# Kernel optimization log

Measured on AMD Instinct MI355X. Metric: run time of the kernel, lower is better.

## Reference

```python
import jax, jax.numpy as jnp
import numpy as np

E = 8      # num_expert
D = 1024   # d_model
H = 2048   # expert hidden (htoh4 size)
K = 2      # top_k
N = 2048   # tokens (batch*seq)


def setup_inputs() -> dict:
    key = jax.random.key(0)
    ks = jax.random.split(key, 4)
    sc = lambda k, shape, s: jax.random.normal(k, shape, jnp.float32) * s
    return {
        "inp": jax.random.normal(ks[0], (N, D), jnp.float32),
        "Wg": sc(ks[1], (D, E), D ** -0.5),          # NaiveGate linear
        "bg": jnp.zeros((E,), jnp.float32),
        "W1": sc(ks[2], (E, D, H), D ** -0.5),        # per-expert htoh4
        "b1": jnp.zeros((E, H), jnp.float32),
        "W2": sc(ks[3], (E, H, D), H ** -0.5),        # per-expert h4toh
        "b2": jnp.zeros((E, D), jnp.float32),
    }


def reference(inp, Wg, bg, W1, b1, W2, b2):
    # NaiveGate: linear -> top_k logits -> softmax over the k selected logits
    logits = inp @ Wg + bg                              # [N, E]
    top_val, top_idx = jax.lax.top_k(logits, K)         # [N, K]
    gate_score = jax.nn.softmax(top_val, axis=-1)       # [N, K]

    # Expert grouped compute. Reference computes every expert on every token
    # (exact math, no capacity dropping); combine selects the routed ones.
    h = jax.nn.gelu(jnp.einsum('nd,edh->neh', inp, W1) + b1)   # [N, E, H]
    y = jnp.einsum('neh,ehd->ned', h, W2) + b2                 # [N, E, D]

    # Combine: equivalent to bmm(gate_score[N,1,K], x[N,K,D]) after gather.
    comb = jnp.sum(jax.nn.one_hot(top_idx, E, dtype=inp.dtype)
                   * gate_score[..., None], axis=1)            # [N, E]
    return jnp.einsum('ne,ned->nd', comb, y)                   # [N, D]
```

## Files before the change

### kernel.cpp

```cpp
#include <hip/hip_runtime.h>
#include <math.h>

#define N_TOK 2048
#define DM    1024
#define HD    2048
#define NE    8
#define RMAX  5120
#define TMAX  40
#define KSPL  2

#define GATE_BLKS 512
#define XCVT_BLKS 1024
#define PREP_BLKS (GATE_BLKS + XCVT_BLKS)
#define WCV2_BLKS 512

typedef short short8 __attribute__((ext_vector_type(8)));
typedef unsigned short u16x8 __attribute__((ext_vector_type(8)));
typedef float f32x4  __attribute__((ext_vector_type(4)));

__device__ inline unsigned short f2b(float f) {
  unsigned int u = __float_as_uint(f);
  return (unsigned short)((u + 0x7FFFu + ((u >> 16) & 1u)) >> 16);
}
__device__ inline float b2f(unsigned short s) {
  return __uint_as_float(((unsigned int)s) << 16);
}
__device__ inline void gload_lds16(const void* g, void* l) {
  __builtin_amdgcn_global_load_lds(
      (const __attribute__((address_space(1))) unsigned int*)g,
      (__attribute__((address_space(3))) unsigned int*)l, 16, 0, 0);
}

__global__ __launch_bounds__(256) void prep_kernel(
    const float* __restrict__ inp, const float* __restrict__ Wg,
    const float* __restrict__ bg,
    int* __restrict__ top_idx, float* __restrict__ gate_w,
    unsigned short* __restrict__ Xb) {
  int bid = blockIdx.x;
  if (bid < GATE_BLKS) {
    int wave = threadIdx.x >> 6;
    int lane = threadIdx.x & 63;
    int n = bid * 4 + wave;
    float acc[NE];
#pragma unroll
    for (int e = 0; e < NE; ++e) acc[e] = 0.f;
    const float4* wg4 = reinterpret_cast<const float4*>(Wg);
#pragma unroll
    for (int i = 0; i < DM / 64; ++i) {
      int d = i * 64 + lane;
      float x = inp[n * DM + d];
      float4 w0 = wg4[d * 2 + 0];
      float4 w1 = wg4[d * 2 + 1];
      acc[0] += x * w0.x; acc[1] += x * w0.y; acc[2] += x * w0.z; acc[3] += x * w0.w;
      acc[4] += x * w1.x; acc[5] += x * w1.y; acc[6] += x * w1.z; acc[7] += x * w1.w;
    }
#pragma unroll
    for (int off = 32; off > 0; off >>= 1) {
#pragma unroll
      for (int e = 0; e < NE; ++e) acc[e] += __shfl_xor(acc[e], off);
    }
    if (lane == 0) {
      float v0 = -1e30f, v1 = -1e30f; int i0 = -1, i1 = -1;
#pragma unroll
      for (int e = 0; e < NE; ++e) {
        float v = acc[e] + bg[e];
        if (v > v0)      { v1 = v0; i1 = i0; v0 = v; i0 = e; }
        else if (v > v1) { v1 = v;  i1 = e; }
      }
      float e1 = expf(v1 - v0);
      float s  = 1.f + e1;
      top_idx[n * 2]     = i0;
      top_idx[n * 2 + 1] = i1;
      gate_w[n * 2]      = 1.f / s;
      gate_w[n * 2 + 1]  = e1 / s;
    }
  } else {
    int i = ((bid - GATE_BLKS) * 256 + threadIdx.x) * 8;
    float4 a = *(const float4*)(inp + i);
    float4 b = *(const float4*)(inp + i + 4);
    ushort4 pa, pb;
    pa.x = f2b(a.x); pa.y = f2b(a.y); pa.z = f2b(a.z); pa.w = f2b(a.w);
    pb.x = f2b(b.x); pb.y = f2b(b.y); pb.z = f2b(b.z); pb.w = f2b(b.w);
    *(ushort4*)(Xb + i)     = pa;
    *(ushort4*)(Xb + i + 4) = pb;
  }
}

__global__ __launch_bounds__(1024) void group_kernel(
    const int* __restrict__ top_idx,
    const float* __restrict__ W2,
    int* __restrict__ token_of, int* __restrict__ inv_g,
    int* __restrict__ tile_expert, int* __restrict__ tile_row0,
    int* __restrict__ n_tiles,
    unsigned short* __restrict__ W2C) {
  if (blockIdx.x != 0) {
    int wb = blockIdx.x - 1;
    int z  = wb >> 6;
    int k0 = (wb & 63) * 32;
    const float* src = W2 + (size_t)z * HD * DM;
    unsigned short* dst = W2C + (size_t)z * HD * DM;
    int t  = threadIdx.x;
    int cg = t & 255, kg = t >> 8;
    const float* s = src + (size_t)(k0 + kg * 8) * DM + cg * 4;
    float4 v[8];
#pragma unroll
    for (int i = 0; i < 8; ++i) v[i] = *(const float4*)(s + (size_t)i * DM);
#pragma unroll
    for (int c = 0; c < 4; ++c) {
      u16x8 o;
      o[0] = f2b(v[0][c]); o[1] = f2b(v[1][c]); o[2] = f2b(v[2][c]); o[3] = f2b(v[3][c]);
      o[4] = f2b(v[4][c]); o[5] = f2b(v[5][c]); o[6] = f2b(v[6][c]); o[7] = f2b(v[7][c]);
      *(u16x8*)(dst + ((size_t)(k0 / 8 + kg) * DM + cg * 4 + c) * 8) = o;
    }
    return;
  }
  __shared__ int s_wtot[16];
  int tid = threadIdx.x, lane = tid & 63, wid = tid >> 6;
  int base = 0, tiles = 0;
  for (int e = 0; e < NE; ++e) {
    int cnt = 0;
#pragma unroll
    for (int c0 = 0; c0 < N_TOK; c0 += 1024) {
      int n = c0 + tid;
      int t0 = top_idx[n * 2], t1 = top_idx[n * 2 + 1];
      bool f = (t0 == e) || (t1 == e);
      int k = (t0 == e) ? 0 : 1;
      unsigned long long m = __ballot(f);
      int lp = __popcll(m & ((1ull << lane) - 1ull));
      if (lane == 0) s_wtot[wid] = __popcll(m);
      __syncthreads();
      int wbase = 0, tot = 0;
#pragma unroll
      for (int w = 0; w < 16; ++w) {
        int c = s_wtot[w];
        if (w < wid) wbase += c;
        tot += c;
      }
      if (f) {
        int pos = base + cnt + wbase + lp;
        token_of[pos] = n;
        inv_g[n * 2 + k] = pos;
      }
      cnt += tot;
      __syncthreads();
    }
    int padded = (cnt + 127) & ~127;
    for (int i = cnt + tid; i < padded; i += 1024) token_of[base + i] = -1;
    if (tid == 0) {
      for (int t = 0; t < padded / 128; ++t) {
        tile_expert[tiles + t] = e;
        tile_row0[tiles + t]   = base + t * 128;
      }
    }
    tiles += padded / 128;
    base  += padded;
    __syncthreads();
  }
  if (tid == 0) n_tiles[0] = tiles;
}

__global__ __launch_bounds__(256, 6) void ffn1_mfma(
    const unsigned short* __restrict__ Xb,
    const float* __restrict__ W1,
    const float* __restrict__ b1,
    const unsigned short* __restrict__ Xzero,
    const int* __restrict__ token_of, const int* __restrict__ tile_expert,
    const int* __restrict__ tile_row0, const int* __restrict__ n_tiles,
    unsigned short* __restrict__ Hbuf) {
  int lin  = blockIdx.x;
  int xcd  = lin & 7, slot = lin >> 3;
  int unit = xcd * 4 + slot / TMAX;
  int t    = slot % TMAX;
  if (t >= n_tiles[0]) return;
  int e    = tile_expert[t];
  int row0 = tile_row0[t];
  int h0   = unit * 64;
  __shared__ __align__(16) unsigned short Asl[2][128][32];
  __shared__ __align__(16) unsigned short Bsl[2][4][64][8];
  int tid = threadIdx.x, lane = tid & 63;
  int wid = tid >> 6, wr = wid >> 1, wc = wid & 1;
  int l15 = lane & 15, l4 = lane >> 4;
  int sw  = (l15 >> 1) & 3;

  int ar[2], asg[2], tk[2];
#pragma unroll
  for (int q = 0; q < 2; ++q) {
    int idx = tid + q * 256;
    ar[q]  = idx >> 2;
    asg[q] = (idx & 3) ^ ((ar[q] >> 1) & 3);
    tk[q]  = token_of[row0 + ar[q]];
  }
  int bcol = tid & 63, bks = tid >> 6;
  const float* W1e = W1 + (size_t)e * DM * HD;

  f32x4 acc[4][2] = {};
  float bvA[8], bvB[8];

  auto issueB = [&](int tt, float* bv) {
    const float* p = W1e + (size_t)(tt * 32 + bks * 8) * HD + h0 + bcol;
#pragma unroll
    for (int i = 0; i < 8; ++i) bv[i] = p[(size_t)i * HD];
  };
  auto packwrite = [&](const float* bv, int buf) {
    u16x8 o;
#pragma unroll
    for (int i = 0; i < 8; ++i) o[i] = f2b(bv[i]);
    *(u16x8*)&Bsl[buf][bks][bcol][0] = o;
  };
  auto issueA = [&](int tt, int buf) {
#pragma unroll
    for (int q = 0; q < 2; ++q) {
      int idx = tid + q * 256;
      const unsigned short* ga = (tk[q] < 0)
          ? Xzero
          : Xb + (size_t)tk[q] * DM + tt * 32 + asg[q] * 8;
      gload_lds16(ga, (char*)&Asl[buf][0][0] + (size_t)idx * 16);
    }
  };
  auto compute = [&](int buf) {
    short8 a[4], b[2];
#pragma unroll
    for (int m = 0; m < 4; ++m) {
      int R = wr * 64 + m * 16 + l15;
      a[m] = *(const short8*)((const char*)&Asl[buf][0][0] + R * 64 + ((l4 ^ sw) << 4));
    }
#pragma unroll
    for (int n = 0; n < 2; ++n)
      b[n] = *(const short8*)&Bsl[buf][l4][wc * 32 + n * 16 + l15][0];
#pragma unroll
    for (int m = 0; m < 4; ++m)
#pragma unroll
      for (int n = 0; n < 2; ++n)
        acc[m][n] = __builtin_amdgcn_mfma_f32_16x16x32_bf16(a[m], b[n], acc[m][n], 0, 0, 0);
  };

  issueB(0, bvA);
  issueA(0, 0);
  for (int kt = 0; kt < 32; kt += 2) {
    packwrite(bvA, 0);
    __syncthreads();
    if (kt + 1 < 32) { issueB(kt + 1, bvB); issueA(kt + 1, 1); }
    compute(0);
    packwrite(bvB, 1);
    __syncthreads();
    if (kt + 2 < 32) { issueB(kt + 2, bvA); issueA(kt + 2, 0); }
    compute(1);
  }

  float bias[2];
#pragma unroll
  for (int n = 0; n < 2; ++n) bias[n] = b1[e * HD + h0 + wc * 32 + n * 16 + l15];
#pragma unroll
  for (int m = 0; m < 4; ++m) {
#pragma unroll
    for (int n = 0; n < 2; ++n) {
      int col = h0 + wc * 32 + n * 16 + l15;
#pragma unroll
      for (int j = 0; j < 4; ++j) {
        int row = row0 + wr * 64 + m * 16 + l4 * 4 + j;
        float x = acc[m][n][j] + bias[n];
        float g = 0.5f * x * (1.f + tanhf(0.7978845608f * (x + 0.044715f * x * x * x)));
        Hbuf[(size_t)row * HD + col] = f2b(g);
      }
    }
  }
}

__global__ __launch_bounds__(256, 6) void ffn2_mfma(
    const unsigned short* __restrict__ Hbuf,
    const unsigned short* __restrict__ W2C,
    const float* __restrict__ b2,
    const int* __restrict__ tile_expert, const int* __restrict__ tile_row0,
    const int* __restrict__ n_tiles,
    float* __restrict__ Ypart) {
  int lin  = blockIdx.x;
  int xcd  = lin & 7, slot = lin >> 3;
  int unit = xcd * 4 + slot / TMAX;
  int t    = slot % TMAX;
  if (t >= n_tiles[0]) return;
  int e    = tile_expert[t];
  int row0 = tile_row0[t];
  int d0   = (unit >> 1) * 64;
  int ks   = unit & 1;
  int kbase = ks * (HD / KSPL);
  int kb0   = kbase >> 3;
  __shared__ __align__(16) unsigned short Asl[2][128][32];
  __shared__ __align__(16) unsigned short Bsl[2][4][64][8];
  int tid = threadIdx.x, lane = tid & 63;
  int wid = tid >> 6, wr = wid >> 1, wc = wid & 1;
  int l15 = lane & 15, l4 = lane >> 4;
  int sw  = (l15 >> 1) & 3;

  int ar[2], asg[2];
#pragma unroll
  for (int q = 0; q < 2; ++q) {
    int idx = tid + q * 256;
    ar[q]  = idx >> 2;
    asg[q] = (idx & 3) ^ ((ar[q] >> 1) & 3);
  }
  int bcol = tid & 63, bks = tid >> 6;
  const unsigned short* W2e = W2C + (size_t)e * HD * DM;

  f32x4 acc[4][2] = {};

  auto issueAB = [&](int tt, int buf) {
#pragma unroll
    for (int q = 0; q < 2; ++q) {
      int idx = tid + q * 256;
      const unsigned short* ga =
          Hbuf + (size_t)(row0 + ar[q]) * HD + kbase + tt * 32 + asg[q] * 8;
      gload_lds16(ga, (char*)&Asl[buf][0][0] + (size_t)idx * 16);
    }
    const unsigned short* gb =
        W2e + ((size_t)(kb0 + tt * 4 + bks) * DM + d0 + bcol) * 8;
    gload_lds16(gb, (char*)&Bsl[buf][0][0] + (size_t)tid * 16);
  };
  auto compute = [&](int buf) {
    short8 a[4], b[2];
#pragma unroll
    for (int m = 0; m < 4; ++m) {
      int R = wr * 64 + m * 16 + l15;
      a[m] = *(const short8*)((const char*)&Asl[buf][0][0] + R * 64 + ((l4 ^ sw) << 4));
    }
#pragma unroll
    for (int n = 0; n < 2; ++n)
      b[n] = *(const short8*)&Bsl[buf][l4][wc * 32 + n * 16 + l15][0];
#pragma unroll
    for (int m = 0; m < 4; ++m)
#pragma unroll
      for (int n = 0; n < 2; ++n)
        acc[m][n] = __builtin_amdgcn_mfma_f32_16x16x32_bf16(a[m], b[n], acc[m][n], 0, 0, 0);
  };

  const int NT = HD / KSPL / 32;
  issueAB(0, 0);
  for (int kt = 0; kt < NT; kt += 2) {
    __syncthreads();
    if (kt + 1 < NT) issueAB(kt + 1, 1);
    compute(0);
    __syncthreads();
    if (kt + 2 < NT) issueAB(kt + 2, 0);
    compute(1);
  }

  float bias[2];
#pragma unroll
  for (int n = 0; n < 2; ++n)
    bias[n] = (ks == 0) ? b2[e * DM + d0 + wc * 32 + n * 16 + l15] : 0.f;
  float* Yp = Ypart + (size_t)ks * RMAX * DM;
#pragma unroll
  for (int m = 0; m < 4; ++m) {
#pragma unroll
    for (int n = 0; n < 2; ++n) {
      int col = d0 + wc * 32 + n * 16 + l15;
#pragma unroll
      for (int j = 0; j < 4; ++j) {
        int row = row0 + wr * 64 + m * 16 + l4 * 4 + j;
        Yp[(size_t)row * DM + col] = acc[m][n][j] + bias[n];
      }
    }
  }
}

__global__ void combine_kernel(const float* __restrict__ Ypart,
                               const int* __restrict__ inv_g,
                               const float* __restrict__ gate_w,
                               float* __restrict__ out) {
  int n = blockIdx.x;
  int r0 = inv_g[n * 2], r1 = inv_g[n * 2 + 1];
  float g0 = gate_w[n * 2], g1 = gate_w[n * 2 + 1];
  int i = threadIdx.x;
  const float4* y00 = (const float4*)(Ypart + (size_t)r0 * DM);
  const float4* y01 = (const float4*)(Ypart + (size_t)(RMAX + r0) * DM);
  const float4* y10 = (const float4*)(Ypart + (size_t)r1 * DM);
  const float4* y11 = (const float4*)(Ypart + (size_t)(RMAX + r1) * DM);
  float4 a0 = y00[i], a1 = y01[i], b0 = y10[i], b1 = y11[i];
  float4 rv;
  rv.x = g0 * (a0.x + a1.x) + g1 * (b0.x + b1.x);
  rv.y = g0 * (a0.y + a1.y) + g1 * (b0.y + b1.y);
  rv.z = g0 * (a0.z + a1.z) + g1 * (b0.z + b1.z);
  rv.w = g0 * (a0.w + a1.w) + g1 * (b0.w + b1.w);
  *(float4*)(out + (size_t)n * DM + i * 4) = rv;
}

extern "C" void kernel_launch(void* const* d_in, const int* in_sizes, int n_in,
                              void* d_out, int out_size, void* d_ws, size_t ws_size,
                              hipStream_t stream) {
  const float* inp = (const float*)d_in[0];
  const float* Wg  = (const float*)d_in[1];
  const float* bg  = (const float*)d_in[2];
  const float* W1  = (const float*)d_in[3];
  const float* b1  = (const float*)d_in[4];
  const float* W2  = (const float*)d_in[5];
  const float* b2  = (const float*)d_in[6];
  float* out = (float*)d_out;

  char* ws = (char*)d_ws;
  size_t off = 0;
  auto alloc = [&](size_t bytes) {
    size_t o = off;
    off = (off + bytes + 255) & ~(size_t)255;
    return o;
  };
  int*   top_idx     = (int*)  (ws + alloc(N_TOK * 2 * sizeof(int)));
  float* gate_w      = (float*)(ws + alloc(N_TOK * 2 * sizeof(float)));
  int*   token_of    = (int*)  (ws + alloc(RMAX * sizeof(int)));
  int*   inv_g       = (int*)  (ws + alloc(N_TOK * 2 * sizeof(int)));
  int*   tile_expert = (int*)  (ws + alloc(TMAX * sizeof(int)));
  int*   tile_row0   = (int*)  (ws + alloc(TMAX * sizeof(int)));
  int*   n_tiles     = (int*)  (ws + alloc(sizeof(int)));
  unsigned short* Xzero = (unsigned short*)(ws + alloc(DM * 2));
  unsigned short* Xb    = (unsigned short*)(ws + alloc((size_t)N_TOK * DM * 2));
  unsigned short* W2C   = (unsigned short*)(ws + alloc((size_t)NE * HD * DM * 2));
  unsigned short* Hbuf  = (unsigned short*)(ws + alloc((size_t)RMAX * HD * 2));
  float*          Ypart = (float*)(ws + alloc((size_t)KSPL * RMAX * DM * 4));
  (void)ws_size;

  hipMemsetAsync(Xzero, 0, DM * 2, stream);
  prep_kernel<<<PREP_BLKS, 256, 0, stream>>>(inp, Wg, bg, top_idx, gate_w, Xb);
  group_kernel<<<1 + WCV2_BLKS, 1024, 0, stream>>>(
      top_idx, W2, token_of, inv_g, tile_expert, tile_row0, n_tiles, W2C);
  ffn1_mfma<<<8 * 4 * TMAX, 256, 0, stream>>>(
      Xb, W1, b1, Xzero, token_of, tile_expert, tile_row0, n_tiles, Hbuf);
  ffn2_mfma<<<8 * 4 * TMAX, 256, 0, stream>>>(
      Hbuf, W2C, b2, tile_expert, tile_row0, n_tiles, Ypart);
  combine_kernel<<<N_TOK, 256, 0, stream>>>(Ypart, inv_g, gate_w, out);
}
```

Before: 137.4 us.

## Pre-convert W1 to packed bf16 and load it via direct-to-LDS loads in ffn1

W1 is now converted once per call to a k-packed bf16 layout inside the group kernel, sharing the path already used for W2. ffn1 then streams B tiles with global_load_lds directly into LDS, as it does for A, instead of doing strided fp32 register loads and converting in the loop. This removes redundant fp32 reads and per-tile conversion across the many blocks that read each expert's weights, and simplifies the main loop. The cost is an extra 64MB fp32 read plus a 32MB bf16 write per call, and more blocks in the group kernel.

```diff
diff --git a/kernel.cpp b/kernel.cpp
--- a/kernel.cpp
+++ b/kernel.cpp
@@ -13,6 +13,7 @@
 #define XCVT_BLKS 1024
 #define PREP_BLKS (GATE_BLKS + XCVT_BLKS)
 #define WCV2_BLKS 512
+#define WCV1_BLKS 512
 
 typedef short short8 __attribute__((ext_vector_type(8)));
 typedef unsigned short u16x8 __attribute__((ext_vector_type(8)));
@@ -88,29 +89,37 @@
 
 __global__ __launch_bounds__(1024) void group_kernel(
     const int* __restrict__ top_idx,
-    const float* __restrict__ W2,
+    const float* __restrict__ W1, const float* __restrict__ W2,
     int* __restrict__ token_of, int* __restrict__ inv_g,
     int* __restrict__ tile_expert, int* __restrict__ tile_row0,
     int* __restrict__ n_tiles,
-    unsigned short* __restrict__ W2C) {
+    unsigned short* __restrict__ W1C, unsigned short* __restrict__ W2C) {
   if (blockIdx.x != 0) {
     int wb = blockIdx.x - 1;
-    int z  = wb >> 6;
-    int k0 = (wb & 63) * 32;
-    const float* src = W2 + (size_t)z * HD * DM;
-    unsigned short* dst = W2C + (size_t)z * HD * DM;
+    const float* src; unsigned short* dst; int N, n0, k0;
+    if (wb < WCV2_BLKS) {
+      int z = wb >> 6;
+      src = W2 + (size_t)z * HD * DM; dst = W2C + (size_t)z * HD * DM;
+      N = DM; n0 = 0; k0 = (wb & 63) * 32;
+    } else {
+      int w1 = wb - WCV2_BLKS;
+      int z = w1 >> 6;
+      int r = w1 & 63;
+      src = W1 + (size_t)z * DM * HD; dst = W1C + (size_t)z * DM * HD;
+      N = HD; n0 = (r & 1) * 1024; k0 = (r >> 1) * 32;
+    }
     int t  = threadIdx.x;
     int cg = t & 255, kg = t >> 8;
-    const float* s = src + (size_t)(k0 + kg * 8) * DM + cg * 4;
+    const float* s = src + (size_t)(k0 + kg * 8) * N + n0 + cg * 4;
     float4 v[8];
 #pragma unroll
-    for (int i = 0; i < 8; ++i) v[i] = *(const float4*)(s + (size_t)i * DM);
+    for (int i = 0; i < 8; ++i) v[i] = *(const float4*)(s + (size_t)i * N);
 #pragma unroll
     for (int c = 0; c < 4; ++c) {
       u16x8 o;
       o[0] = f2b(v[0][c]); o[1] = f2b(v[1][c]); o[2] = f2b(v[2][c]); o[3] = f2b(v[3][c]);
       o[4] = f2b(v[4][c]); o[5] = f2b(v[5][c]); o[6] = f2b(v[6][c]); o[7] = f2b(v[7][c]);
-      *(u16x8*)(dst + ((size_t)(k0 / 8 + kg) * DM + cg * 4 + c) * 8) = o;
+      *(u16x8*)(dst + ((size_t)(k0 / 8 + kg) * N + n0 + cg * 4 + c) * 8) = o;
     }
     return;
   }
@@ -161,7 +170,7 @@
 
 __global__ __launch_bounds__(256, 6) void ffn1_mfma(
     const unsigned short* __restrict__ Xb,
-    const float* __restrict__ W1,
+    const unsigned short* __restrict__ W1C,
     const float* __restrict__ b1,
     const unsigned short* __restrict__ Xzero,
     const int* __restrict__ token_of, const int* __restrict__ tile_expert,
@@ -191,23 +200,11 @@
     tk[q]  = token_of[row0 + ar[q]];
   }
   int bcol = tid & 63, bks = tid >> 6;
-  const float* W1e = W1 + (size_t)e * DM * HD;
+  const unsigned short* W1e = W1C + (size_t)e * DM * HD;
 
   f32x4 acc[4][2] = {};
-  float bvA[8], bvB[8];
-
-  auto issueB = [&](int tt, float* bv) {
-    const float* p = W1e + (size_t)(tt * 32 + bks * 8) * HD + h0 + bcol;
-#pragma unroll
-    for (int i = 0; i < 8; ++i) bv[i] = p[(size_t)i * HD];
-  };
-  auto packwrite = [&](const float* bv, int buf) {
-    u16x8 o;
-#pragma unroll
-    for (int i = 0; i < 8; ++i) o[i] = f2b(bv[i]);
-    *(u16x8*)&Bsl[buf][bks][bcol][0] = o;
-  };
-  auto issueA = [&](int tt, int buf) {
+
+  auto issueAB = [&](int tt, int buf) {
 #pragma unroll
     for (int q = 0; q < 2; ++q) {
       int idx = tid + q * 256;
@@ -216,6 +213,9 @@
           : Xb + (size_t)tk[q] * DM + tt * 32 + asg[q] * 8;
       gload_lds16(ga, (char*)&Asl[buf][0][0] + (size_t)idx * 16);
     }
+    const unsigned short* gb =
+        W1e + ((size_t)(tt * 4 + bks) * HD + h0 + bcol) * 8;
+    gload_lds16(gb, (char*)&Bsl[buf][0][0] + (size_t)tid * 16);
   };
   auto compute = [&](int buf) {
     short8 a[4], b[2];
@@ -234,16 +234,13 @@
         acc[m][n] = __builtin_amdgcn_mfma_f32_16x16x32_bf16(a[m], b[n], acc[m][n], 0, 0, 0);
   };
 
-  issueB(0, bvA);
-  issueA(0, 0);
+  issueAB(0, 0);
   for (int kt = 0; kt < 32; kt += 2) {
-    packwrite(bvA, 0);
     __syncthreads();
-    if (kt + 1 < 32) { issueB(kt + 1, bvB); issueA(kt + 1, 1); }
+    if (kt + 1 < 32) issueAB(kt + 1, 1);
     compute(0);
-    packwrite(bvB, 1);
     __syncthreads();
-    if (kt + 2 < 32) { issueB(kt + 2, bvA); issueA(kt + 2, 0); }
+    if (kt + 2 < 32) issueAB(kt + 2, 0);
     compute(1);
   }
 
@@ -411,6 +408,7 @@
   int*   n_tiles     = (int*)  (ws + alloc(sizeof(int)));
   unsigned short* Xzero = (unsigned short*)(ws + alloc(DM * 2));
   unsigned short* Xb    = (unsigned short*)(ws + alloc((size_t)N_TOK * DM * 2));
+  unsigned short* W1C   = (unsigned short*)(ws + alloc((size_t)NE * DM * HD * 2));
   unsigned short* W2C   = (unsigned short*)(ws + alloc((size_t)NE * HD * DM * 2));
   unsigned short* Hbuf  = (unsigned short*)(ws + alloc((size_t)RMAX * HD * 2));
   float*          Ypart = (float*)(ws + alloc((size_t)KSPL * RMAX * DM * 4));
@@ -418,10 +416,11 @@
 
   hipMemsetAsync(Xzero, 0, DM * 2, stream);
   prep_kernel<<<PREP_BLKS, 256, 0, stream>>>(inp, Wg, bg, top_idx, gate_w, Xb);
-  group_kernel<<<1 + WCV2_BLKS, 1024, 0, stream>>>(
-      top_idx, W2, token_of, inv_g, tile_expert, tile_row0, n_tiles, W2C);
+  group_kernel<<<1 + WCV2_BLKS + WCV1_BLKS, 1024, 0, stream>>>(
+      top_idx, W1, W2, token_of, inv_g, tile_expert, tile_row0, n_tiles,
+      W1C, W2C);
   ffn1_mfma<<<8 * 4 * TMAX, 256, 0, stream>>>(
-      Xb, W1, b1, Xzero, token_of, tile_expert, tile_row0, n_tiles, Hbuf);
+      Xb, W1C, b1, Xzero, token_of, tile_expert, tile_row0, n_tiles, Hbuf);
   ffn2_mfma<<<8 * 4 * TMAX, 256, 0, stream>>>(
       Hbuf, W2C, b2, tile_expert, tile_row0, n_tiles, Ypart);
   combine_kernel<<<N_TOK, 256, 0, stream>>>(Ypart, inv_g, gate_w, out);
```

After: 145.5 us. 5.9% more time.

## Load fp32 W1 tiles directly to LDS and convert to bf16 at fragment read

Applied to the files above, without the earlier changes.

The W1 path in ffn1 stops loading 8 strided fp32 values per thread into registers, converting them to bf16 and writing them to LDS. It instead issues direct global-to-LDS 16-byte loads of the raw fp32 tile, using a swizzled layout, and converts to bf16 when each wave reads its B fragments. This removes the register staging and the separate pack/write step, and lets the B loads use the same async path as A. In exchange LDS use for B doubles, the bf16 conversion is repeated by every wave that reads the fragment, fragment reads become 8 scalar LDS reads, and launch bounds drop to 5 waves.

```diff
diff --git a/kernel.cpp b/kernel.cpp
--- a/kernel.cpp
+++ b/kernel.cpp
@@ -159,7 +159,7 @@
   if (tid == 0) n_tiles[0] = tiles;
 }
 
-__global__ __launch_bounds__(256, 6) void ffn1_mfma(
+__global__ __launch_bounds__(256, 5) void ffn1_mfma(
     const unsigned short* __restrict__ Xb,
     const float* __restrict__ W1,
     const float* __restrict__ b1,
@@ -176,7 +176,7 @@
   int row0 = tile_row0[t];
   int h0   = unit * 64;
   __shared__ __align__(16) unsigned short Asl[2][128][32];
-  __shared__ __align__(16) unsigned short Bsl[2][4][64][8];
+  __shared__ __align__(16) float Bsl[2][32][64];
   int tid = threadIdx.x, lane = tid & 63;
   int wid = tid >> 6, wr = wid >> 1, wc = wid & 1;
   int l15 = lane & 15, l4 = lane >> 4;
@@ -190,24 +190,18 @@
     asg[q] = (idx & 3) ^ ((ar[q] >> 1) & 3);
     tk[q]  = token_of[row0 + ar[q]];
   }
-  int bcol = tid & 63, bks = tid >> 6;
+  int bk[2], bc[2];
+#pragma unroll
+  for (int q = 0; q < 2; ++q) {
+    int o = tid + q * 256;
+    bk[q] = o >> 4;
+    bc[q] = (o & 15) ^ ((bk[q] >> 3) << 2);
+  }
   const float* W1e = W1 + (size_t)e * DM * HD;
 
   f32x4 acc[4][2] = {};
-  float bvA[8], bvB[8];
-
-  auto issueB = [&](int tt, float* bv) {
-    const float* p = W1e + (size_t)(tt * 32 + bks * 8) * HD + h0 + bcol;
-#pragma unroll
-    for (int i = 0; i < 8; ++i) bv[i] = p[(size_t)i * HD];
-  };
-  auto packwrite = [&](const float* bv, int buf) {
-    u16x8 o;
-#pragma unroll
-    for (int i = 0; i < 8; ++i) o[i] = f2b(bv[i]);
-    *(u16x8*)&Bsl[buf][bks][bcol][0] = o;
-  };
-  auto issueA = [&](int tt, int buf) {
+
+  auto issueAB = [&](int tt, int buf) {
 #pragma unroll
     for (int q = 0; q < 2; ++q) {
       int idx = tid + q * 256;
@@ -216,6 +210,12 @@
           : Xb + (size_t)tk[q] * DM + tt * 32 + asg[q] * 8;
       gload_lds16(ga, (char*)&Asl[buf][0][0] + (size_t)idx * 16);
     }
+#pragma unroll
+    for (int q = 0; q < 2; ++q) {
+      int o = tid + q * 256;
+      const float* gb = W1e + (size_t)(tt * 32 + bk[q]) * HD + h0 + bc[q] * 4;
+      gload_lds16(gb, (char*)&Bsl[buf][0][0] + (size_t)o * 16);
+    }
   };
   auto compute = [&](int buf) {
     short8 a[4], b[2];
@@ -225,8 +225,15 @@
       a[m] = *(const short8*)((const char*)&Asl[buf][0][0] + R * 64 + ((l4 ^ sw) << 4));
     }
 #pragma unroll
-    for (int n = 0; n < 2; ++n)
-      b[n] = *(const short8*)&Bsl[buf][l4][wc * 32 + n * 16 + l15][0];
+    for (int n = 0; n < 2; ++n) {
+      int col = wc * 32 + n * 16 + l15;
+      int cw  = (((col >> 2) ^ (l4 << 2)) << 2) + (col & 3);
+      short8 bb;
+#pragma unroll
+      for (int i = 0; i < 8; ++i)
+        bb[i] = (short)f2b(Bsl[buf][l4 * 8 + i][cw]);
+      b[n] = bb;
+    }
 #pragma unroll
     for (int m = 0; m < 4; ++m)
 #pragma unroll
@@ -234,16 +241,13 @@
         acc[m][n] = __builtin_amdgcn_mfma_f32_16x16x32_bf16(a[m], b[n], acc[m][n], 0, 0, 0);
   };
 
-  issueB(0, bvA);
-  issueA(0, 0);
+  issueAB(0, 0);
   for (int kt = 0; kt < 32; kt += 2) {
-    packwrite(bvA, 0);
     __syncthreads();
-    if (kt + 1 < 32) { issueB(kt + 1, bvB); issueA(kt + 1, 1); }
+    if (kt + 1 < 32) issueAB(kt + 1, 1);
     compute(0);
-    packwrite(bvB, 1);
     __syncthreads();
-    if (kt + 2 < 32) { issueB(kt + 2, bvA); issueA(kt + 2, 0); }
+    if (kt + 2 < 32) issueAB(kt + 2, 0);
     compute(1);
   }
 
```

After: 152.8 us. 1.11x slower.
